# Kernel optimization log

Measured on AMD Instinct MI355X. Metric: run time of the kernel, lower is better.

The kernel has to match this reference:

```python
import jax, jax.numpy as jnp
import numpy as np

THRESH = 0.5     # confidence threshold (forward arg 'thresh' in the original)
IOU_THR = 0.1    # nms(boxes, 0.1) in the original
K = 512          # fixed top-k candidates per scale (static-shape stand-in for nonzero())


def _decode(output, anchors, stride, k):
    """Filter + parse for one scale. output: [B, 3*(5+nc), H, W]."""
    B, C, H, W = output.shape
    o = output.transpose(0, 2, 3, 1).reshape(B, H, W, 3, -1)   # [B,H,W,3,5+nc]
    D = o.shape[-1]
    conf = jax.nn.sigmoid(o[..., 0]).reshape(-1)               # [B*H*W*3]
    scores, idx = jax.lax.top_k(conf, k)                       # fixed-size filter
    n, h, w, a = jnp.unravel_index(idx, (B, H, W, 3))
    v = o.reshape(-1, D)[idx]                                  # [K, 5+nc]
    dt = v.dtype
    cy = (h.astype(dt) + jax.nn.sigmoid(v[:, 2])) * stride
    cx = (w.astype(dt) + jax.nn.sigmoid(v[:, 1])) * stride
    bw = anchors[a, 0] * jnp.exp(v[:, 3])
    bh = anchors[a, 1] * jnp.exp(v[:, 4])
    cond = jax.nn.sigmoid(v[:, 0])
    cls = jnp.argmax(v[:, 5:], axis=1).astype(dt)              # argmax(softmax)=argmax
    boxes = jnp.stack([n.astype(dt), cond, cx, cy, bw, bh, cls], axis=1)  # [K,7]
    valid = cond > THRESH
    return boxes, valid


def _nms(boxes, valid, iou_thr):
    """Greedy per-image, per-class NMS. boxes: [N,7] = (n, cond, cx, cy, w, h, cls)."""
    N = boxes.shape[0]
    score = jnp.where(valid, boxes[:, 1], -jnp.inf)
    order = jnp.argsort(-score)
    b = boxes[order]
    val = valid[order]
    x1 = b[:, 2] - b[:, 4] * 0.5
    y1 = b[:, 3] - b[:, 5] * 0.5
    x2 = b[:, 2] + b[:, 4] * 0.5
    y2 = b[:, 3] + b[:, 5] * 0.5
    area = b[:, 4] * b[:, 5]
    ix1 = jnp.maximum(x1[:, None], x1[None, :])
    iy1 = jnp.maximum(y1[:, None], y1[None, :])
    ix2 = jnp.minimum(x2[:, None], x2[None, :])
    iy2 = jnp.minimum(y2[:, None], y2[None, :])
    inter = jnp.clip(ix2 - ix1, 0) * jnp.clip(iy2 - iy1, 0)
    iou = inter / (area[:, None] + area[None, :] - inter + 1e-9)
    same = (b[:, 0, None] == b[None, :, 0]) & (b[:, 6, None] == b[None, :, 6])
    overlap = (iou > iou_thr) & same                           # [N,N] bool, no grad needed
    rng = jnp.arange(N)

    def body(i, supp):
        row = overlap[i] & (rng > i)
        active = (~supp[i]) & val[i]
        return jnp.where(active, supp | row, supp)

    supp = jax.lax.fori_loop(0, N, body, jnp.zeros(N, bool))
    keep = val & (~supp)
    return b * keep[:, None].astype(b.dtype), keep


def setup_inputs() -> dict:
    key = jax.random.key(0)
    ks = jax.random.split(key, 6)
    B, C = 64, 255  # 3 * (5 + 80 classes)
    return {
        "output_13": jax.random.normal(ks[0], (B, C, 13, 13), jnp.float32),
        "output_26": jax.random.normal(ks[1], (B, C, 26, 26), jnp.float32),
        "output_52": jax.random.normal(ks[2], (B, C, 52, 52), jnp.float32),
        "anchors_13": jax.random.uniform(ks[3], (3, 2), jnp.float32, 90.0, 330.0),
        "anchors_26": jax.random.uniform(ks[4], (3, 2), jnp.float32, 30.0, 120.0),
        "anchors_52": jax.random.uniform(ks[5], (3, 2), jnp.float32, 10.0, 60.0),
    }


def reference(output_13, output_26, output_52, anchors_13, anchors_26, anchors_52):
    b13, v13 = _decode(output_13, anchors_13, 32.0, K)
    b26, v26 = _decode(output_26, anchors_26, 16.0, K)
    b52, v52 = _decode(output_52, anchors_52, 8.0, K)
    boxes = jnp.concatenate([b13, b26, b52], axis=0)   # [3K, 7]
    valid = jnp.concatenate([v13, v26, v52], axis=0)
    final_boxes, keep = _nms(boxes, valid, IOU_THR)
    return final_boxes, keep
```

## Files before the change

kernel.cpp:

```cpp
#include <hip/hip_runtime.h>
#include <stdint.h>

#define K_SEL 512
#define NBOX 1536
#define CAND_CAP 4096
#define HBITS 13
#define HBINS 8192
#define NSHARD 128
#define SEG 128
#define HBLK 64
#define HB0 8
#define HB1 16
#define HB2 40
#define ICAP 56

#define M0 32448
#define M1 129792
#define M2 519168
#define M_TOT (M0+M1+M2)

#define OFF_HIST 0u
#define OFF_CNT  98304u
#define OFF_THR  99840u
#define OFF_CAND 99872u
#define OFF_BOX  493088u
#define OFF_SKEY 536096u
#define OFF_TOPK 548384u
#define ZERO_BYTES 99840u

typedef unsigned long long u64;
typedef uint32_t u32;
typedef uint16_t u16;

__device__ __forceinline__ float sigf(float x) { return 1.0f / (1.0f + expf(-x)); }

__device__ __forceinline__ u32 fmono(float f) {
    u32 u = __float_as_uint(f);
    return (u & 0x80000000u) ? ~u : (u | 0x80000000u);
}

__global__ __launch_bounds__(1024) void k_hist(const float* p0, const float* p1, const float* p2,
                                               uint8_t* ws) {
    __shared__ u32 lh[HBINS];
    for (int i = threadIdx.x; i < HBINS; i += 1024) lh[i] = 0;
    __syncthreads();
    int b = blockIdx.x, s, b0, nb;
    if (b < HB0)            { s = 0; b0 = b;             nb = HB0; }
    else if (b < HB0 + HB1) { s = 1; b0 = b - HB0;       nb = HB1; }
    else                    { s = 2; b0 = b - HB0 - HB1; nb = HB2; }
    int M = (s == 0) ? M0 : (s == 1) ? M1 : M2;
    int H = (s == 0) ? 13 : (s == 1) ? 26 : 52;
    int HW = H * H;
    const float* p = (s == 0) ? p0 : (s == 1) ? p1 : p2;
    for (int o = b0 * 1024 + threadIdx.x; o < M; o += nb * 1024) {
        int n = o / (3 * HW); int rem = o - n * 3 * HW;
        int a = rem / HW;     int pix = rem - a * HW;
        float conf = sigf(p[(size_t)(n * 255 + a * 85) * HW + pix]);
        atomicAdd(&lh[fmono(conf) >> (32 - HBITS)], 1u);
    }
    __syncthreads();
    u32* gh = (u32*)(ws + OFF_HIST) + s * HBINS;
    for (int i = threadIdx.x; i < HBINS; i += 1024) {
        u32 v = lh[i];
        if (v) atomicAdd(&gh[i], v);
    }
}

__global__ __launch_bounds__(1024) void k_scan(uint8_t* ws) {
    int s = blockIdx.x;
    u32* hist = (u32*)(ws + OFF_HIST) + s * HBINS;
    __shared__ u32 sum[1024];
    int t = threadIdx.x;
    u32 bins[8];
    const uint4* hp = (const uint4*)(hist + t * 8);
    uint4 x = hp[0], y = hp[1];
    bins[0] = x.x; bins[1] = x.y; bins[2] = x.z; bins[3] = x.w;
    bins[4] = y.x; bins[5] = y.y; bins[6] = y.z; bins[7] = y.w;
    u32 acc = 0;
#pragma unroll
    for (int k = 0; k < 8; ++k) acc += bins[k];
    sum[t] = acc;
    __syncthreads();
    for (int off = 1; off < 1024; off <<= 1) {
        u32 v = (t + off < 1024) ? sum[t + off] : 0;
        __syncthreads();
        sum[t] += v;
        __syncthreads();
    }
    u32 excl = (t < 1023) ? sum[t + 1] : 0;
    u32 mine = sum[t] - excl;
    if (excl < K_SEL && excl + mine >= K_SEL) {
        u32 cum = excl; int thr = t * 8;
#pragma unroll
        for (int k = 7; k >= 0; --k) {
            cum += bins[k];
            if (cum >= K_SEL) { thr = t * 8 + k; break; }
        }
        ((u32*)(ws + OFF_THR))[s] = (u32)thr;
    }
}

__global__ __launch_bounds__(1024) void k_compact(const float* p0, const float* p1, const float* p2,
                                                  uint8_t* ws) {
    int t = blockIdx.x * 1024 + threadIdx.x;
    if (t >= M_TOT) return;
    int s, o, H;
    if (t < M0)            { s = 0; o = t;           H = 13; }
    else if (t < M0 + M1)  { s = 1; o = t - M0;      H = 26; }
    else                   { s = 2; o = t - M0 - M1; H = 52; }
    const float* p = (s == 0) ? p0 : (s == 1) ? p1 : p2;
    int HW = H * H;
    int n = o / (3 * HW); int rem = o - n * 3 * HW;
    int a = rem / HW;     int pix = rem - a * HW;
    float conf = sigf(p[(size_t)(n * 255 + a * 85) * HW + pix]);
    u32 cb = fmono(conf);
    if ((cb >> (32 - HBITS)) >= ((u32*)(ws + OFF_THR))[s]) {
        int c = n * (3 * HW) + pix * 3 + a;
        int idx = s * NSHARD + (blockIdx.x & (NSHARD - 1));
        u32 pos = atomicAdd(&((u32*)(ws + OFF_CNT))[idx], 1u);
        if (pos < SEG) {
            u64 key = ((u64)cb << 32) | (u32)(~(u32)c);
            ((u64*)(ws + OFF_CAND))[(u32)idx * SEG + pos] = key;
        }
    }
}

__global__ __launch_bounds__(1024) void k_sortsel(uint8_t* ws) {
    int s = blockIdx.x;
    __shared__ u64 a_[CAND_CAP];
    __shared__ u32 scnt[NSHARD], spre[NSHARD];
    __shared__ u32 total_s;
    int t = threadIdx.x;
    if (t < NSHARD) {
        u32 v = ((u32*)(ws + OFF_CNT))[s * NSHARD + t];
        scnt[t] = (v > SEG) ? SEG : v;
        spre[t] = scnt[t];
    }
    __syncthreads();
    for (int off = 1; off < NSHARD; off <<= 1) {
        u32 v = (t >= off && t < NSHARD) ? spre[t - off] : 0;
        __syncthreads();
        if (t < NSHARD) spre[t] += v;
        __syncthreads();
    }
    if (t == 0) total_s = (spre[NSHARD - 1] > CAND_CAP) ? CAND_CAP : spre[NSHARD - 1];
    __syncthreads();
    u32 total = total_s;
    int n2 = K_SEL;
    while (n2 < (int)total) n2 <<= 1;
    for (int i = t; i < n2; i += 1024) a_[i] = 0ull;
    __syncthreads();
    if (t < NSHARD) {
        u32 base = spre[t] - scnt[t];
        const u64* seg = (const u64*)(ws + OFF_CAND) + (u32)(s * NSHARD + t) * SEG;
        for (u32 i = 0; i < scnt[t]; ++i)
            if (base + i < CAND_CAP) a_[base + i] = seg[i];
    }
    __syncthreads();
    for (int k = 2; k <= n2; k <<= 1) {
        for (int j = k >> 1; j > 0; j >>= 1) {
            for (int i = t; i < n2; i += 1024) {
                int ixj = i ^ j;
                if (ixj > i) {
                    bool desc = ((i & k) == 0);
                    u64 x = a_[i], y = a_[ixj];
                    if (desc ? (x < y) : (x > y)) { a_[i] = y; a_[ixj] = x; }
                }
            }
            __syncthreads();
        }
    }
    u64* topk = (u64*)(ws + OFF_TOPK) + s * K_SEL;
    for (int r = t; r < K_SEL; r += 1024) topk[r] = a_[r];
}

__global__ __launch_bounds__(1024) void k_decode(const float* p0, const float* p1, const float* p2,
                                                 const float* a0, const float* a1, const float* a2,
                                                 uint8_t* ws) {
    int t = blockIdx.x * 1024 + threadIdx.x;
    int g = t >> 4, l = t & 15;
    if (g >= NBOX) return;
    int s = g >> 9, r = g & 511;
    int H = (s == 0) ? 13 : (s == 1) ? 26 : 52;
    float stride = (s == 0) ? 32.f : (s == 1) ? 16.f : 8.f;
    const float* p    = (s == 0) ? p0 : (s == 1) ? p1 : p2;
    const float* anch = (s == 0) ? a0 : (s == 1) ? a1 : a2;
    int HW = H * H, hw3 = HW * 3;
    u64 key = ((u64*)(ws + OFF_TOPK))[g];
    int c = (int)(~(u32)key);
    int n = c / hw3; int rem = c - n * hw3;
    int pix = rem / 3; int aa = rem - pix * 3;
    size_t base = (size_t)(n * 255 + aa * 85) * HW + pix;
    float best = -INFINITY; int bi = 0x7FFFFFFF;
#pragma unroll
    for (int m = 0; m < 5; ++m) {
        int k2 = l + m * 16;
        float vv = p[base + (size_t)(5 + k2) * HW];
        if (vv > best) { best = vv; bi = k2; }
    }
    float vload = (l < 5) ? p[base + (size_t)l * HW] : 0.f;
#pragma unroll
    for (int off = 8; off > 0; off >>= 1) {
        float ov = __shfl_down(best, off, 16);
        int oi = __shfl_down(bi, off, 16);
        if (ov > best || (ov == best && oi < bi)) { best = ov; bi = oi; }
    }
    float v0 = __shfl(vload, 0, 16);
    float v1 = __shfl(vload, 1, 16);
    float v2 = __shfl(vload, 2, 16);
    float v3 = __shfl(vload, 3, 16);
    float v4 = __shfl(vload, 4, 16);
    if (l == 0) {
        int h = pix / H, w = pix - h * H;
        float conf = sigf(v0);
        float cx = ((float)w + sigf(v1)) * stride;
        float cy = ((float)h + sigf(v2)) * stride;
        float bw = anch[aa * 2 + 0] * expf(v3);
        float bh = anch[aa * 2 + 1] * expf(v4);
        float* box = (float*)(ws + OFF_BOX) + g * 7;
        box[0] = (float)n; box[1] = conf; box[2] = cx; box[3] = cy;
        box[4] = bw; box[5] = bh; box[6] = (float)bi;
        u32 mono = (conf > 0.5f) ? fmono(conf) : fmono(-INFINITY);
        ((u64*)(ws + OFF_SKEY))[g] = ((u64)mono << 32) | (u32)(~(u32)g);
    }
}

__global__ __launch_bounds__(1024) void k_tail(uint8_t* ws, float* out) {
    __shared__ u64 sk[NBOX];
    __shared__ u16 srt[NBOX];
    __shared__ float gx1[NBOX], gy1[NBOX], gx2[NBOX], gy2[NBOX], gar[NBOX];
    __shared__ u32 meta[NBOX];
    __shared__ uint8_t gkeep[NBOX];
    __shared__ u16 lists[64 * ICAP];
    __shared__ u32 icnt[64];
    u32* wvcnt = (u32*)sk;
    int t = threadIdx.x;
    u64* skey = (u64*)(ws + OFF_SKEY);
    for (int i = t; i < NBOX; i += 1024) sk[i] = skey[i];
    __syncthreads();
    for (int i = t; i < NBOX; i += 1024) {
        int s = i >> 9, r = i & 511;
        u64 K = sk[i];
        int g = r;
#pragma unroll
        for (int s2 = 0; s2 < 3; ++s2) {
            if (s2 == s) continue;
            const u64* seg = &sk[s2 << 9];
            int lo = 0, hi = 512;
            while (lo < hi) {
                int mid = (lo + hi) >> 1;
                if (seg[mid] > K) lo = mid + 1; else hi = mid;
            }
            g += lo;
        }
        srt[g] = (u16)i;
    }
    __syncthreads();
    const float* box = (const float*)(ws + OFF_BOX);
    for (int i = t; i < NBOX; i += 1024) {
        int pos = srt[i];
        float b0 = box[pos * 7 + 0], b1 = box[pos * 7 + 1], b2 = box[pos * 7 + 2];
        float b3 = box[pos * 7 + 3], b4 = box[pos * 7 + 4], b5 = box[pos * 7 + 5];
        float b6 = box[pos * 7 + 6];
        gx1[i] = b2 - b4 * 0.5f;  gy1[i] = b3 - b5 * 0.5f;
        gx2[i] = b2 + b4 * 0.5f;  gy2[i] = b3 + b5 * 0.5f;
        gar[i] = b4 * b5;
        meta[i] = (u32)(int)b0 | ((u32)(int)b6 << 8) | ((b1 > 0.5f) ? (1u << 16) : 0u);
        gkeep[i] = 0;
        wvcnt[i] = 0;
    }
    __syncthreads();
#pragma unroll
    for (int pass = 0; pass < 2; ++pass) {
        int ii = t + pass * 1024;
        u32 img = (ii < NBOX) ? (meta[ii] & 63u) : 0u;
        u64 mask = ~0ull;
#pragma unroll
        for (int b = 0; b < 6; ++b) {
            bool bit = (img >> b) & 1u;
            u64 bal = __ballot(bit);
            mask &= bit ? bal : ~bal;
        }
        if (ii < NBOX) {
            int lane = ii & 63;
            int wrank = __popcll(mask & ((1ull << lane) - 1ull));
            if (wrank == 0) wvcnt[(ii >> 6) * 64 + img] = (u32)__popcll(mask);
        }
    }
    __syncthreads();
    if (t < 64) {
        u32 c = 0;
        for (int w = 0; w < 24; ++w) c += wvcnt[w * 64 + t];
        icnt[t] = c;
    }
#pragma unroll
    for (int pass = 0; pass < 2; ++pass) {
        int ii = t + pass * 1024;
        u32 img = (ii < NBOX) ? (meta[ii] & 63u) : 0u;
        u64 mask = ~0ull;
#pragma unroll
        for (int b = 0; b < 6; ++b) {
            bool bit = (img >> b) & 1u;
            u64 bal = __ballot(bit);
            mask &= bit ? bal : ~bal;
        }
        if (ii < NBOX) {
            int lane = ii & 63;
            int wv = ii >> 6;
            int r = __popcll(mask & ((1ull << lane) - 1ull));
            for (int w = 0; w < wv; ++w) r += (int)wvcnt[w * 64 + img];
            if (r < ICAP) lists[img * ICAP + r] = (u16)ii;
        }
    }
    __syncthreads();
    {
        int wv = t >> 6, lane = t & 63;
        for (int im = wv * 4; im < wv * 4 + 4; ++im) {
            int cnt = (int)icnt[im]; if (cnt > ICAP) cnt = ICAP;
            float x1 = 0, y1 = 0, x2 = 0, y2 = 0, ar = 0;
            u32 cl = 0; int u = -1; bool val = false;
            if (lane < cnt) {
                u = lists[im * ICAP + lane];
                x1 = gx1[u]; y1 = gy1[u]; x2 = gx2[u]; y2 = gy2[u]; ar = gar[u];
                u32 m = meta[u]; cl = (m >> 8) & 0xFFu; val = (m >> 16) & 1u;
            }
            u64 valmask = __ballot(val);
            u64 keptmask = 0;
            for (int a = 0; a < cnt; ++a) {
                float ax1 = __shfl(x1, a), ay1 = __shfl(y1, a);
                float ax2 = __shfl(x2, a), ay2 = __shfl(y2, a);
                float aar = __shfl(ar, a);
                u32 acl = (u32)__shfl((int)cl, a);
                float ix1 = fmaxf(x1, ax1), iy1 = fmaxf(y1, ay1);
                float ix2 = fminf(x2, ax2), iy2 = fminf(y2, ay2);
                float iw = fmaxf(ix2 - ix1, 0.f), ih = fmaxf(iy2 - iy1, 0.f);
                float inter = iw * ih;
                float iou = inter / (ar + aar - inter + 1e-9f);
                bool viol = (lane < a) && ((keptmask >> lane) & 1ull) &&
                            (cl == acl) && (iou > 0.1f);
                u64 bal = __ballot(viol);
                bool kept = ((valmask >> a) & 1ull) && (bal == 0ull);
                if (kept) keptmask |= (1ull << a);
            }
            if (lane < cnt) gkeep[u] = (uint8_t)((keptmask >> lane) & 1ull);
        }
    }
    __syncthreads();
    for (int i = t; i < NBOX; i += 1024) {
        float kf = gkeep[i] ? 1.f : 0.f;
        int pos = srt[i];
        for (int k = 0; k < 7; ++k) out[i * 7 + k] = box[pos * 7 + k] * kf;
        out[NBOX * 7 + i] = kf;
    }
}

extern "C" void kernel_launch(void* const* d_in, const int* in_sizes, int n_in,
                              void* d_out, int out_size, void* d_ws, size_t ws_size,
                              hipStream_t stream) {
    const float* p0 = (const float*)d_in[0];
    const float* p1 = (const float*)d_in[1];
    const float* p2 = (const float*)d_in[2];
    const float* a0 = (const float*)d_in[3];
    const float* a1 = (const float*)d_in[4];
    const float* a2 = (const float*)d_in[5];
    uint8_t* ws = (uint8_t*)d_ws;
    float* out = (float*)d_out;

    const int CB = (M_TOT + 1023) / 1024;

    hipMemsetAsync(ws, 0, ZERO_BYTES, stream);
    k_hist   <<<HBLK, 1024, 0, stream>>>(p0, p1, p2, ws);
    k_scan   <<<3, 1024, 0, stream>>>(ws);
    k_compact<<<CB, 1024, 0, stream>>>(p0, p1, p2, ws);
    k_sortsel<<<3, 1024, 0, stream>>>(ws);
    k_decode <<<24, 1024, 0, stream>>>(p0, p1, p2, a0, a1, a2, ws);
    k_tail   <<<1, 1024, 0, stream>>>(ws, out);
}
```

Measured before the change: 118.0 us.

## Fuse top-k sort with decode, use register wave bitonic sort, drop memset

The pipeline now writes per-block histogram slices, which k_scan sums, in place of global atomics. Shard counters are zeroed inside k_scan, so the memset launch goes away. The shared-memory bitonic sort and the separate decode kernel are merged into one kernel. Each of 8 waves sorts 512 keys in registers with shuffles, and a merge tree keeps the top 512. Every one of the 24 blocks redundantly re-sorts its scale's candidates and then decodes its own 64 boxes, trading duplicated sort work for fewer launches and shorter barrier chains. The histogram block count is also cut from 64 to 24.

```diff
diff --git a/kernel.cpp b/kernel.cpp
--- a/kernel.cpp
+++ b/kernel.cpp
@@ -3,15 +3,11 @@
 
 #define K_SEL 512
 #define NBOX 1536
-#define CAND_CAP 4096
 #define HBITS 13
 #define HBINS 8192
 #define NSHARD 128
 #define SEG 128
-#define HBLK 64
-#define HB0 8
-#define HB1 16
-#define HB2 40
+#define HBLK 24
 #define ICAP 56
 
 #define M0 32448
@@ -19,14 +15,12 @@
 #define M2 519168
 #define M_TOT (M0+M1+M2)
 
-#define OFF_HIST 0u
-#define OFF_CNT  98304u
-#define OFF_THR  99840u
-#define OFF_CAND 99872u
-#define OFF_BOX  493088u
-#define OFF_SKEY 536096u
-#define OFF_TOPK 548384u
-#define ZERO_BYTES 99840u
+#define OFF_HSL  0u
+#define OFF_CNT  786432u
+#define OFF_THR  787968u
+#define OFF_CAND 788000u
+#define OFF_BOX  1181216u
+#define OFF_SKEY 1224224u
 
 typedef unsigned long long u64;
 typedef uint32_t u32;
@@ -37,6 +31,69 @@
 __device__ __forceinline__ u32 fmono(float f) {
     u32 u = __float_as_uint(f);
     return (u & 0x80000000u) ? ~u : (u | 0x80000000u);
+}
+
+__device__ __forceinline__ u64 sx64(u64 v, int m) {
+    int lo = __shfl_xor((int)(u32)v, m);
+    int hi = __shfl_xor((int)(v >> 32), m);
+    return ((u64)(u32)hi << 32) | (u32)lo;
+}
+
+__device__ __forceinline__ void ce_reg(u64& lo, u64& hi, bool desc) {
+    u64 mx = lo > hi ? lo : hi;
+    u64 mn = lo > hi ? hi : lo;
+    lo = desc ? mx : mn;
+    hi = desc ? mn : mx;
+}
+
+__device__ __forceinline__ void wave_sort512(u64 (&kr)[8], int lane) {
+#pragma unroll
+    for (int k = 2; k <= 512; k <<= 1) {
+#pragma unroll
+        for (int j = k >> 1; j > 0; j >>= 1) {
+            if (j >= 64) {
+                int rj = j >> 6;
+#pragma unroll
+                for (int r = 0; r < 8; ++r) {
+                    if ((r & rj) == 0) {
+                        bool desc = ((r & (k >> 6)) == 0);
+                        ce_reg(kr[r], kr[r | rj], desc);
+                    }
+                }
+            } else {
+#pragma unroll
+                for (int r = 0; r < 8; ++r) {
+                    u64 other = sx64(kr[r], j);
+                    bool desc = (k < 64) ? ((lane & k) == 0) : ((r & (k >> 6)) == 0);
+                    bool keep_max = (((lane & j) == 0) == desc);
+                    u64 mx = kr[r] > other ? kr[r] : other;
+                    u64 mn = kr[r] > other ? other : kr[r];
+                    kr[r] = keep_max ? mx : mn;
+                }
+            }
+        }
+    }
+}
+
+__device__ __forceinline__ void wave_clean512(u64 (&kr)[8], int lane) {
+#pragma unroll
+    for (int j = 256; j > 0; j >>= 1) {
+        if (j >= 64) {
+            int rj = j >> 6;
+#pragma unroll
+            for (int r = 0; r < 8; ++r)
+                if ((r & rj) == 0) ce_reg(kr[r], kr[r | rj], true);
+        } else {
+#pragma unroll
+            for (int r = 0; r < 8; ++r) {
+                u64 other = sx64(kr[r], j);
+                bool keep_max = ((lane & j) == 0);
+                u64 mx = kr[r] > other ? kr[r] : other;
+                u64 mn = kr[r] > other ? other : kr[r];
+                kr[r] = keep_max ? mx : mn;
+            }
+        }
+    }
 }
 
 __global__ __launch_bounds__(1024) void k_hist(const float* p0, const float* p1, const float* p2,
@@ -45,9 +102,9 @@
     for (int i = threadIdx.x; i < HBINS; i += 1024) lh[i] = 0;
     __syncthreads();
     int b = blockIdx.x, s, b0, nb;
-    if (b < HB0)            { s = 0; b0 = b;             nb = HB0; }
-    else if (b < HB0 + HB1) { s = 1; b0 = b - HB0;       nb = HB1; }
-    else                    { s = 2; b0 = b - HB0 - HB1; nb = HB2; }
+    if (b < 2)      { s = 0; b0 = b;     nb = 2;  }
+    else if (b < 8) { s = 1; b0 = b - 2; nb = 6;  }
+    else            { s = 2; b0 = b - 8; nb = 16; }
     int M = (s == 0) ? M0 : (s == 1) ? M1 : M2;
     int H = (s == 0) ? 13 : (s == 1) ? 26 : 52;
     int HW = H * H;
@@ -59,23 +116,26 @@
         atomicAdd(&lh[fmono(conf) >> (32 - HBITS)], 1u);
     }
     __syncthreads();
-    u32* gh = (u32*)(ws + OFF_HIST) + s * HBINS;
-    for (int i = threadIdx.x; i < HBINS; i += 1024) {
-        u32 v = lh[i];
-        if (v) atomicAdd(&gh[i], v);
-    }
+    u32* slice = (u32*)(ws + OFF_HSL) + (u32)b * HBINS;
+    for (int i = threadIdx.x; i < HBINS; i += 1024) slice[i] = lh[i];
 }
 
 __global__ __launch_bounds__(1024) void k_scan(uint8_t* ws) {
     int s = blockIdx.x;
-    u32* hist = (u32*)(ws + OFF_HIST) + s * HBINS;
+    int b0 = (s == 0) ? 0 : (s == 1) ? 2 : 8;
+    int b1 = (s == 0) ? 2 : (s == 1) ? 8 : 24;
     __shared__ u32 sum[1024];
     int t = threadIdx.x;
+    if (t < NSHARD) ((u32*)(ws + OFF_CNT))[s * NSHARD + t] = 0;
     u32 bins[8];
-    const uint4* hp = (const uint4*)(hist + t * 8);
-    uint4 x = hp[0], y = hp[1];
-    bins[0] = x.x; bins[1] = x.y; bins[2] = x.z; bins[3] = x.w;
-    bins[4] = y.x; bins[5] = y.y; bins[6] = y.z; bins[7] = y.w;
+#pragma unroll
+    for (int k = 0; k < 8; ++k) bins[k] = 0;
+    for (int b = b0; b < b1; ++b) {
+        const uint4* sl = (const uint4*)((u32*)(ws + OFF_HSL) + (u32)b * HBINS + t * 8);
+        uint4 x = sl[0], y = sl[1];
+        bins[0] += x.x; bins[1] += x.y; bins[2] += x.z; bins[3] += x.w;
+        bins[4] += y.x; bins[5] += y.y; bins[6] += y.z; bins[7] += y.w;
+    }
     u32 acc = 0;
 #pragma unroll
     for (int k = 0; k < 8; ++k) acc += bins[k];
@@ -125,11 +185,14 @@
     }
 }
 
-__global__ __launch_bounds__(1024) void k_sortsel(uint8_t* ws) {
-    int s = blockIdx.x;
-    __shared__ u64 a_[CAND_CAP];
+__global__ __launch_bounds__(1024) void k_sortdec(const float* p0, const float* p1, const float* p2,
+                                                  const float* a0, const float* a1, const float* a2,
+                                                  uint8_t* ws) {
+    int s = blockIdx.x >> 3, sub = blockIdx.x & 7;
+    __shared__ u64 a_[4096];
     __shared__ u32 scnt[NSHARD], spre[NSHARD];
-    __shared__ u32 total_s;
+    __shared__ float pbv[64];
+    __shared__ int pbi[64];
     int t = threadIdx.x;
     if (t < NSHARD) {
         u32 v = ((u32*)(ws + OFF_CNT))[s * NSHARD + t];
@@ -143,50 +206,84 @@
         if (t < NSHARD) spre[t] += v;
         __syncthreads();
     }
-    if (t == 0) total_s = (spre[NSHARD - 1] > CAND_CAP) ? CAND_CAP : spre[NSHARD - 1];
-    __syncthreads();
-    u32 total = total_s;
-    int n2 = K_SEL;
-    while (n2 < (int)total) n2 <<= 1;
-    for (int i = t; i < n2; i += 1024) a_[i] = 0ull;
+    for (int i = t; i < 4096; i += 1024) a_[i] = 0ull;
     __syncthreads();
     if (t < NSHARD) {
         u32 base = spre[t] - scnt[t];
         const u64* seg = (const u64*)(ws + OFF_CAND) + (u32)(s * NSHARD + t) * SEG;
         for (u32 i = 0; i < scnt[t]; ++i)
-            if (base + i < CAND_CAP) a_[base + i] = seg[i];
-    }
-    __syncthreads();
-    for (int k = 2; k <= n2; k <<= 1) {
-        for (int j = k >> 1; j > 0; j >>= 1) {
-            for (int i = t; i < n2; i += 1024) {
-                int ixj = i ^ j;
-                if (ixj > i) {
-                    bool desc = ((i & k) == 0);
-                    u64 x = a_[i], y = a_[ixj];
-                    if (desc ? (x < y) : (x > y)) { a_[i] = y; a_[ixj] = x; }
-                }
-            }
-            __syncthreads();
-        }
-    }
-    u64* topk = (u64*)(ws + OFF_TOPK) + s * K_SEL;
-    for (int r = t; r < K_SEL; r += 1024) topk[r] = a_[r];
-}
-
-__global__ __launch_bounds__(1024) void k_decode(const float* p0, const float* p1, const float* p2,
-                                                 const float* a0, const float* a1, const float* a2,
-                                                 uint8_t* ws) {
-    int t = blockIdx.x * 1024 + threadIdx.x;
-    int g = t >> 4, l = t & 15;
-    if (g >= NBOX) return;
-    int s = g >> 9, r = g & 511;
+            if (base + i < 4096) a_[base + i] = seg[i];
+    }
+    __syncthreads();
+    int wv = t >> 6, lane = t & 63;
+    u64 kr[8];
+    if (wv < 8) {
+#pragma unroll
+        for (int r = 0; r < 8; ++r) kr[r] = a_[wv * 512 + r * 64 + lane];
+        wave_sort512(kr, lane);
+    }
+    __syncthreads();
+    if (wv < 8) {
+#pragma unroll
+        for (int r = 0; r < 8; ++r) a_[wv * 512 + r * 64 + lane] = kr[r];
+    }
+    __syncthreads();
+    if (wv < 4) {
+#pragma unroll
+        for (int r = 0; r < 8; ++r) {
+            int e = r * 64 + lane;
+            u64 A = a_[(2 * wv) * 512 + e];
+            u64 B = a_[(2 * wv + 1) * 512 + 511 - e];
+            kr[r] = A > B ? A : B;
+        }
+        wave_clean512(kr, lane);
+    }
+    __syncthreads();
+    if (wv < 4) {
+#pragma unroll
+        for (int r = 0; r < 8; ++r) a_[wv * 512 + r * 64 + lane] = kr[r];
+    }
+    __syncthreads();
+    if (wv < 2) {
+#pragma unroll
+        for (int r = 0; r < 8; ++r) {
+            int e = r * 64 + lane;
+            u64 A = a_[(2 * wv) * 512 + e];
+            u64 B = a_[(2 * wv + 1) * 512 + 511 - e];
+            kr[r] = A > B ? A : B;
+        }
+        wave_clean512(kr, lane);
+    }
+    __syncthreads();
+    if (wv < 2) {
+#pragma unroll
+        for (int r = 0; r < 8; ++r) a_[wv * 512 + r * 64 + lane] = kr[r];
+    }
+    __syncthreads();
+    if (wv == 0) {
+#pragma unroll
+        for (int r = 0; r < 8; ++r) {
+            int e = r * 64 + lane;
+            u64 A = a_[e];
+            u64 B = a_[512 + 511 - e];
+            kr[r] = A > B ? A : B;
+        }
+        wave_clean512(kr, lane);
+    }
+    __syncthreads();
+    if (wv == 0) {
+#pragma unroll
+        for (int r = 0; r < 8; ++r) a_[r * 64 + lane] = kr[r];
+    }
+    __syncthreads();
+    int g16 = t >> 4, l = t & 15;
+    int rloc = sub * 64 + g16;
     int H = (s == 0) ? 13 : (s == 1) ? 26 : 52;
     float stride = (s == 0) ? 32.f : (s == 1) ? 16.f : 8.f;
     const float* p    = (s == 0) ? p0 : (s == 1) ? p1 : p2;
     const float* anch = (s == 0) ? a0 : (s == 1) ? a1 : a2;
     int HW = H * H, hw3 = HW * 3;
-    u64 key = ((u64*)(ws + OFF_TOPK))[g];
+    u64 key = a_[rloc];
     int c = (int)(~(u32)key);
     int n = c / hw3; int rem = c - n * hw3;
     int pix = rem / 3; int aa = rem - pix * 3;
@@ -210,6 +307,7 @@
     float v2 = __shfl(vload, 2, 16);
     float v3 = __shfl(vload, 3, 16);
     float v4 = __shfl(vload, 4, 16);
+    (void)pbv; (void)pbi;
     if (l == 0) {
         int h = pix / H, w = pix - h * H;
         float conf = sigf(v0);
@@ -217,11 +315,12 @@
         float cy = ((float)h + sigf(v2)) * stride;
         float bw = anch[aa * 2 + 0] * expf(v3);
         float bh = anch[aa * 2 + 1] * expf(v4);
-        float* box = (float*)(ws + OFF_BOX) + g * 7;
+        int gi = s * K_SEL + rloc;
+        float* box = (float*)(ws + OFF_BOX) + gi * 7;
         box[0] = (float)n; box[1] = conf; box[2] = cx; box[3] = cy;
         box[4] = bw; box[5] = bh; box[6] = (float)bi;
         u32 mono = (conf > 0.5f) ? fmono(conf) : fmono(-INFINITY);
-        ((u64*)(ws + OFF_SKEY))[g] = ((u64)mono << 32) | (u32)(~(u32)g);
+        ((u64*)(ws + OFF_SKEY))[gi] = ((u64)mono << 32) | (u32)(~(u32)gi);
     }
 }
 
@@ -368,11 +467,9 @@
 
     const int CB = (M_TOT + 1023) / 1024;
 
-    hipMemsetAsync(ws, 0, ZERO_BYTES, stream);
     k_hist   <<<HBLK, 1024, 0, stream>>>(p0, p1, p2, ws);
     k_scan   <<<3, 1024, 0, stream>>>(ws);
     k_compact<<<CB, 1024, 0, stream>>>(p0, p1, p2, ws);
-    k_sortsel<<<3, 1024, 0, stream>>>(ws);
-    k_decode <<<24, 1024, 0, stream>>>(p0, p1, p2, a0, a1, a2, ws);
+    k_sortdec<<<24, 1024, 0, stream>>>(p0, p1, p2, a0, a1, a2, ws);
     k_tail   <<<1, 1024, 0, stream>>>(ws, out);
 }
```

After: 125.2 us. 6.1% more time.

## Fuse all stages into one cooperative persistent kernel with grid syncs

Applied to the files above, without the earlier changes.

Replaces the memset and six separate launches with a single cooperative kernel of 192 blocks that runs histogram, scan, compaction, sort, decode and NMS tail as phases separated by grid-wide syncs, with shared memory held in a union. Histogram blocks now write per-block slices that the scan reduces, so global atomics and the memset go away. Compaction becomes a grid-stride loop. A multi-kernel fallback remains for when the cooperative launch fails. The aim is to remove launch and inter-kernel gaps, at the cost of grid-sync overhead, fewer histogram blocks, and mostly idle blocks during the serial phases.

```diff
diff --git a/kernel.cpp b/kernel.cpp
--- a/kernel.cpp
+++ b/kernel.cpp
@@ -1,17 +1,17 @@
 #include <hip/hip_runtime.h>
+#include <hip/hip_cooperative_groups.h>
 #include <stdint.h>
 
+namespace cg = cooperative_groups;
+
+#define GRID 192
 #define K_SEL 512
 #define NBOX 1536
-#define CAND_CAP 4096
 #define HBITS 13
 #define HBINS 8192
 #define NSHARD 128
 #define SEG 128
-#define HBLK 64
-#define HB0 8
-#define HB1 16
-#define HB2 40
+#define HBLK 24
 #define ICAP 56
 
 #define M0 32448
@@ -19,14 +19,13 @@
 #define M2 519168
 #define M_TOT (M0+M1+M2)
 
-#define OFF_HIST 0u
-#define OFF_CNT  98304u
-#define OFF_THR  99840u
-#define OFF_CAND 99872u
-#define OFF_BOX  493088u
-#define OFF_SKEY 536096u
-#define OFF_TOPK 548384u
-#define ZERO_BYTES 99840u
+#define OFF_HSL  0u
+#define OFF_CNT  786432u
+#define OFF_THR  787968u
+#define OFF_CAND 788000u
+#define OFF_BOX  1181216u
+#define OFF_SKEY 1224224u
+#define OFF_TOPK 1236512u
 
 typedef unsigned long long u64;
 typedef uint32_t u32;
@@ -39,43 +38,61 @@
     return (u & 0x80000000u) ? ~u : (u | 0x80000000u);
 }
 
-__global__ __launch_bounds__(1024) void k_hist(const float* p0, const float* p1, const float* p2,
-                                               uint8_t* ws) {
-    __shared__ u32 lh[HBINS];
-    for (int i = threadIdx.x; i < HBINS; i += 1024) lh[i] = 0;
-    __syncthreads();
-    int b = blockIdx.x, s, b0, nb;
-    if (b < HB0)            { s = 0; b0 = b;             nb = HB0; }
-    else if (b < HB0 + HB1) { s = 1; b0 = b - HB0;       nb = HB1; }
-    else                    { s = 2; b0 = b - HB0 - HB1; nb = HB2; }
+struct SortSh {
+    u64 a_[4096];
+    u32 scnt[NSHARD], spre[NSHARD];
+};
+struct TailSh {
+    u64 sk[NBOX];
+    u16 srt[NBOX];
+    float gx1[NBOX], gy1[NBOX], gx2[NBOX], gy2[NBOX], gar[NBOX];
+    u32 meta[NBOX];
+    uint8_t gkeep[NBOX];
+    u16 lists[64 * ICAP];
+    u32 icnt[64];
+};
+union AllSh {
+    u32 lh[HBINS];
+    u32 sum[1024];
+    SortSh sort;
+    TailSh tail;
+};
+
+__device__ void dev_hist(int hb, const float* p0, const float* p1, const float* p2,
+                         uint8_t* ws, u32* lh, int t) {
+    for (int i = t; i < HBINS; i += 1024) lh[i] = 0;
+    __syncthreads();
+    int s, b0, nb;
+    if (hb < 2)      { s = 0; b0 = hb;     nb = 2;  }
+    else if (hb < 8) { s = 1; b0 = hb - 2; nb = 6;  }
+    else             { s = 2; b0 = hb - 8; nb = 16; }
     int M = (s == 0) ? M0 : (s == 1) ? M1 : M2;
     int H = (s == 0) ? 13 : (s == 1) ? 26 : 52;
     int HW = H * H;
     const float* p = (s == 0) ? p0 : (s == 1) ? p1 : p2;
-    for (int o = b0 * 1024 + threadIdx.x; o < M; o += nb * 1024) {
+    for (int o = b0 * 1024 + t; o < M; o += nb * 1024) {
         int n = o / (3 * HW); int rem = o - n * 3 * HW;
         int a = rem / HW;     int pix = rem - a * HW;
         float conf = sigf(p[(size_t)(n * 255 + a * 85) * HW + pix]);
         atomicAdd(&lh[fmono(conf) >> (32 - HBITS)], 1u);
     }
     __syncthreads();
-    u32* gh = (u32*)(ws + OFF_HIST) + s * HBINS;
-    for (int i = threadIdx.x; i < HBINS; i += 1024) {
-        u32 v = lh[i];
-        if (v) atomicAdd(&gh[i], v);
-    }
-}
-
-__global__ __launch_bounds__(1024) void k_scan(uint8_t* ws) {
-    int s = blockIdx.x;
-    u32* hist = (u32*)(ws + OFF_HIST) + s * HBINS;
-    __shared__ u32 sum[1024];
-    int t = threadIdx.x;
+    u32* slice = (u32*)(ws + OFF_HSL) + (u32)hb * HBINS;
+    for (int i = t; i < HBINS; i += 1024) slice[i] = lh[i];
+}
+
+__device__ void dev_scan(int s, uint8_t* ws, u32* sum, int t) {
+    int b0 = (s == 0) ? 0 : (s == 1) ? 2 : 8;
+    int b1 = (s == 0) ? 2 : (s == 1) ? 8 : 24;
     u32 bins[8];
-    const uint4* hp = (const uint4*)(hist + t * 8);
-    uint4 x = hp[0], y = hp[1];
-    bins[0] = x.x; bins[1] = x.y; bins[2] = x.z; bins[3] = x.w;
-    bins[4] = y.x; bins[5] = y.y; bins[6] = y.z; bins[7] = y.w;
+#pragma unroll
+    for (int k = 0; k < 8; ++k) bins[k] = 0;
+    for (int b = b0; b < b1; ++b) {
+        const uint4* sl = (const uint4*)((u32*)(ws + OFF_HSL) + (u32)b * HBINS + t * 8);
+        uint4 x = sl[0], y = sl[1];
+        bins[0] += x.x; bins[1] += x.y; bins[2] += x.z; bins[3] += x.w;
+        bins[4] += y.x; bins[5] += y.y; bins[6] += y.z; bins[7] += y.w;
+    }
     u32 acc = 0;
 #pragma unroll
     for (int k = 0; k < 8; ++k) acc += bins[k];
@@ -100,61 +117,56 @@
     }
 }
 
-__global__ __launch_bounds__(1024) void k_compact(const float* p0, const float* p1, const float* p2,
-                                                  uint8_t* ws) {
-    int t = blockIdx.x * 1024 + threadIdx.x;
-    if (t >= M_TOT) return;
-    int s, o, H;
-    if (t < M0)            { s = 0; o = t;           H = 13; }
-    else if (t < M0 + M1)  { s = 1; o = t - M0;      H = 26; }
-    else                   { s = 2; o = t - M0 - M1; H = 52; }
-    const float* p = (s == 0) ? p0 : (s == 1) ? p1 : p2;
-    int HW = H * H;
-    int n = o / (3 * HW); int rem = o - n * 3 * HW;
-    int a = rem / HW;     int pix = rem - a * HW;
-    float conf = sigf(p[(size_t)(n * 255 + a * 85) * HW + pix]);
-    u32 cb = fmono(conf);
-    if ((cb >> (32 - HBITS)) >= ((u32*)(ws + OFF_THR))[s]) {
-        int c = n * (3 * HW) + pix * 3 + a;
-        int idx = s * NSHARD + (blockIdx.x & (NSHARD - 1));
-        u32 pos = atomicAdd(&((u32*)(ws + OFF_CNT))[idx], 1u);
-        if (pos < SEG) {
-            u64 key = ((u64)cb << 32) | (u32)(~(u32)c);
-            ((u64*)(ws + OFF_CAND))[(u32)idx * SEG + pos] = key;
-        }
-    }
-}
-
-__global__ __launch_bounds__(1024) void k_sortsel(uint8_t* ws) {
-    int s = blockIdx.x;
-    __shared__ u64 a_[CAND_CAP];
-    __shared__ u32 scnt[NSHARD], spre[NSHARD];
-    __shared__ u32 total_s;
-    int t = threadIdx.x;
+__device__ void dev_compact(int bid, int t, const float* p0, const float* p1, const float* p2,
+                            uint8_t* ws) {
+    const u32* thr = (const u32*)(ws + OFF_THR);
+    for (int i = bid * 1024 + t; i < M_TOT; i += GRID * 1024) {
+        int s, o, H;
+        if (i < M0)            { s = 0; o = i;           H = 13; }
+        else if (i < M0 + M1)  { s = 1; o = i - M0;      H = 26; }
+        else                   { s = 2; o = i - M0 - M1; H = 52; }
+        const float* p = (s == 0) ? p0 : (s == 1) ? p1 : p2;
+        int HW = H * H;
+        int n = o / (3 * HW); int rem = o - n * 3 * HW;
+        int a = rem / HW;     int pix = rem - a * HW;
+        float conf = sigf(p[(size_t)(n * 255 + a * 85) * HW + pix]);
+        u32 cb = fmono(conf);
+        if ((cb >> (32 - HBITS)) >= thr[s]) {
+            int c = n * (3 * HW) + pix * 3 + a;
+            int idx = s * NSHARD + (bid & (NSHARD - 1));
+            u32 pos = atomicAdd(&((u32*)(ws + OFF_CNT))[idx], 1u);
+            if (pos < SEG) {
+                u64 key = ((u64)cb << 32) | (u32)(~(u32)c);
+                ((u64*)(ws + OFF_CAND))[(u32)idx * SEG + pos] = key;
+            }
+        }
+    }
+}
+
+__device__ void dev_sort(int s, uint8_t* ws, SortSh& S, int t) {
     if (t < NSHARD) {
         u32 v = ((u32*)(ws + OFF_CNT))[s * NSHARD + t];
-        scnt[t] = (v > SEG) ? SEG : v;
-        spre[t] = scnt[t];
+        S.scnt[t] = (v > SEG) ? SEG : v;
+        S.spre[t] = S.scnt[t];
     }
     __syncthreads();
     for (int off = 1; off < NSHARD; off <<= 1) {
-        u32 v = (t >= off && t < NSHARD) ? spre[t - off] : 0;
+        u32 v = (t >= off && t < NSHARD) ? S.spre[t - off] : 0;
         __syncthreads();
-        if (t < NSHARD) spre[t] += v;
+        if (t < NSHARD) S.spre[t] += v;
         __syncthreads();
     }
-    if (t == 0) total_s = (spre[NSHARD - 1] > CAND_CAP) ? CAND_CAP : spre[NSHARD - 1];
-    __syncthreads();
-    u32 total = total_s;
+    u32 total = S.spre[NSHARD - 1];
+    if (total > 4096) total = 4096;
     int n2 = K_SEL;
     while (n2 < (int)total) n2 <<= 1;
-    for (int i = t; i < n2; i += 1024) a_[i] = 0ull;
+    for (int i = t; i < n2; i += 1024) S.a_[i] = 0ull;
     __syncthreads();
     if (t < NSHARD) {
-        u32 base = spre[t] - scnt[t];
+        u32 base = S.spre[t] - S.scnt[t];
         const u64* seg = (const u64*)(ws + OFF_CAND) + (u32)(s * NSHARD + t) * SEG;
-        for (u32 i = 0; i < scnt[t]; ++i)
-            if (base + i < CAND_CAP) a_[base + i] = seg[i];
+        for (u32 i = 0; i < S.scnt[t]; ++i)
+            if (base + i < 4096) S.a_[base + i] = seg[i];
     }
     __syncthreads();
     for (int k = 2; k <= n2; k <<= 1) {
@@ -163,24 +175,21 @@
                 int ixj = i ^ j;
                 if (ixj > i) {
                     bool desc = ((i & k) == 0);
-                    u64 x = a_[i], y = a_[ixj];
-                    if (desc ? (x < y) : (x > y)) { a_[i] = y; a_[ixj] = x; }
+                    u64 x = S.a_[i], y = S.a_[ixj];
+                    if (desc ? (x < y) : (x > y)) { S.a_[i] = y; S.a_[ixj] = x; }
                 }
             }
             __syncthreads();
         }
     }
     u64* topk = (u64*)(ws + OFF_TOPK) + s * K_SEL;
-    for (int r = t; r < K_SEL; r += 1024) topk[r] = a_[r];
-}
-
-__global__ __launch_bounds__(1024) void k_decode(const float* p0, const float* p1, const float* p2,
-                                                 const float* a0, const float* a1, const float* a2,
-                                                 uint8_t* ws) {
-    int t = blockIdx.x * 1024 + threadIdx.x;
-    int g = t >> 4, l = t & 15;
-    if (g >= NBOX) return;
-    int s = g >> 9, r = g & 511;
+    for (int r = t; r < K_SEL; r += 1024) topk[r] = S.a_[r];
+}
+
+__device__ void dev_decode(int g, int l,
+                           const float* p0, const float* p1, const float* p2,
+                           const float* a0, const float* a1, const float* a2, uint8_t* ws) {
+    int s = g >> 9;
     int H = (s == 0) ? 13 : (s == 1) ? 26 : 52;
     float stride = (s == 0) ? 32.f : (s == 1) ? 16.f : 8.f;
     const float* p    = (s == 0) ? p0 : (s == 1) ? p1 : p2;
@@ -225,27 +234,19 @@
     }
 }
 
-__global__ __launch_bounds__(1024) void k_tail(uint8_t* ws, float* out) {
-    __shared__ u64 sk[NBOX];
-    __shared__ u16 srt[NBOX];
-    __shared__ float gx1[NBOX], gy1[NBOX], gx2[NBOX], gy2[NBOX], gar[NBOX];
-    __shared__ u32 meta[NBOX];
-    __shared__ uint8_t gkeep[NBOX];
-    __shared__ u16 lists[64 * ICAP];
-    __shared__ u32 icnt[64];
-    u32* wvcnt = (u32*)sk;
-    int t = threadIdx.x;
+__device__ void dev_tail(uint8_t* ws, float* out, TailSh& T, int t) {
+    u32* wvcnt = (u32*)T.sk;
     u64* skey = (u64*)(ws + OFF_SKEY);
-    for (int i = t; i < NBOX; i += 1024) sk[i] = skey[i];
+    for (int i = t; i < NBOX; i += 1024) T.sk[i] = skey[i];
     __syncthreads();
     for (int i = t; i < NBOX; i += 1024) {
         int s = i >> 9, r = i & 511;
-        u64 K = sk[i];
+        u64 K = T.sk[i];
         int g = r;
 #pragma unroll
         for (int s2 = 0; s2 < 3; ++s2) {
             if (s2 == s) continue;
-            const u64* seg = &sk[s2 << 9];
+            const u64* seg = &T.sk[s2 << 9];
             int lo = 0, hi = 512;
             while (lo < hi) {
                 int mid = (lo + hi) >> 1;
@@ -253,27 +254,27 @@
             }
             g += lo;
         }
-        srt[g] = (u16)i;
+        T.srt[g] = (u16)i;
     }
     __syncthreads();
     const float* box = (const float*)(ws + OFF_BOX);
     for (int i = t; i < NBOX; i += 1024) {
-        int pos = srt[i];
+        int pos = T.srt[i];
         float b0 = box[pos * 7 + 0], b1 = box[pos * 7 + 1], b2 = box[pos * 7 + 2];
         float b3 = box[pos * 7 + 3], b4 = box[pos * 7 + 4], b5 = box[pos * 7 + 5];
         float b6 = box[pos * 7 + 6];
-        gx1[i] = b2 - b4 * 0.5f;  gy1[i] = b3 - b5 * 0.5f;
-        gx2[i] = b2 + b4 * 0.5f;  gy2[i] = b3 + b5 * 0.5f;
-        gar[i] = b4 * b5;
-        meta[i] = (u32)(int)b0 | ((u32)(int)b6 << 8) | ((b1 > 0.5f) ? (1u << 16) : 0u);
-        gkeep[i] = 0;
+        T.gx1[i] = b2 - b4 * 0.5f;  T.gy1[i] = b3 - b5 * 0.5f;
+        T.gx2[i] = b2 + b4 * 0.5f;  T.gy2[i] = b3 + b5 * 0.5f;
+        T.gar[i] = b4 * b5;
+        T.meta[i] = (u32)(int)b0 | ((u32)(int)b6 << 8) | ((b1 > 0.5f) ? (1u << 16) : 0u);
+        T.gkeep[i] = 0;
         wvcnt[i] = 0;
     }
     __syncthreads();
 #pragma unroll
     for (int pass = 0; pass < 2; ++pass) {
         int ii = t + pass * 1024;
-        u32 img = (ii < NBOX) ? (meta[ii] & 63u) : 0u;
+        u32 img = (ii < NBOX) ? (T.meta[ii] & 63u) : 0u;
         u64 mask = ~0ull;
 #pragma unroll
         for (int b = 0; b < 6; ++b) {
@@ -291,12 +292,12 @@
     if (t < 64) {
         u32 c = 0;
         for (int w = 0; w < 24; ++w) c += wvcnt[w * 64 + t];
-        icnt[t] = c;
+        T.icnt[t] = c;
     }
 #pragma unroll
     for (int pass = 0; pass < 2; ++pass) {
         int ii = t + pass * 1024;
-        u32 img = (ii < NBOX) ? (meta[ii] & 63u) : 0u;
+        u32 img = (ii < NBOX) ? (T.meta[ii] & 63u) : 0u;
         u64 mask = ~0ull;
 #pragma unroll
         for (int b = 0; b < 6; ++b) {
@@ -306,23 +307,23 @@
         }
         if (ii < NBOX) {
             int lane = ii & 63;
-            int wv = ii >> 6;
+            int wvv = ii >> 6;
             int r = __popcll(mask & ((1ull << lane) - 1ull));
-            for (int w = 0; w < wv; ++w) r += (int)wvcnt[w * 64 + img];
-            if (r < ICAP) lists[img * ICAP + r] = (u16)ii;
+            for (int w = 0; w < wvv; ++w) r += (int)wvcnt[w * 64 + img];
+            if (r < ICAP) T.lists[img * ICAP + r] = (u16)ii;
         }
     }
     __syncthreads();
     {
         int wv = t >> 6, lane = t & 63;
         for (int im = wv * 4; im < wv * 4 + 4; ++im) {
-            int cnt = (int)icnt[im]; if (cnt > ICAP) cnt = ICAP;
+            int cnt = (int)T.icnt[im]; if (cnt > ICAP) cnt = ICAP;
             float x1 = 0, y1 = 0, x2 = 0, y2 = 0, ar = 0;
             u32 cl = 0; int u = -1; bool val = false;
             if (lane < cnt) {
-                u = lists[im * ICAP + lane];
-                x1 = gx1[u]; y1 = gy1[u]; x2 = gx2[u]; y2 = gy2[u]; ar = gar[u];
-                u32 m = meta[u]; cl = (m >> 8) & 0xFFu; val = (m >> 16) & 1u;
+                u = T.lists[im * ICAP + lane];
+                x1 = T.gx1[u]; y1 = T.gy1[u]; x2 = T.gx2[u]; y2 = T.gy2[u]; ar = T.gar[u];
+                u32 m = T.meta[u]; cl = (m >> 8) & 0xFFu; val = (m >> 16) & 1u;
             }
             u64 valmask = __ballot(val);
             u64 keptmask = 0;
@@ -342,16 +343,71 @@
                 bool kept = ((valmask >> a) & 1ull) && (bal == 0ull);
                 if (kept) keptmask |= (1ull << a);
             }
-            if (lane < cnt) gkeep[u] = (uint8_t)((keptmask >> lane) & 1ull);
+            if (lane < cnt) T.gkeep[u] = (uint8_t)((keptmask >> lane) & 1ull);
         }
     }
     __syncthreads();
     for (int i = t; i < NBOX; i += 1024) {
-        float kf = gkeep[i] ? 1.f : 0.f;
-        int pos = srt[i];
+        float kf = T.gkeep[i] ? 1.f : 0.f;
+        int pos = T.srt[i];
         for (int k = 0; k < 7; ++k) out[i * 7 + k] = box[pos * 7 + k] * kf;
         out[NBOX * 7 + i] = kf;
     }
+}
+
+__global__ __launch_bounds__(1024) void k_all(const float* p0, const float* p1, const float* p2,
+                                              const float* a0, const float* a1, const float* a2,
+                                              uint8_t* ws, float* out) {
+    __shared__ AllSh sh;
+    cg::grid_group grid = cg::this_grid();
+    int bid = blockIdx.x, t = threadIdx.x;
+
+    if (bid < HBLK) dev_hist(bid, p0, p1, p2, ws, sh.lh, t);
+    if (bid == HBLK && t < 3 * NSHARD) ((u32*)(ws + OFF_CNT))[t] = 0;
+    grid.sync();
+
+    if (bid < 3) dev_scan(bid, ws, sh.sum, t);
+    grid.sync();
+
+    dev_compact(bid, t, p0, p1, p2, ws);
+    grid.sync();
+
+    if (bid < 3) dev_sort(bid, ws, sh.sort, t);
+    grid.sync();
+
+    if (t < 128) dev_decode(bid * 8 + (t >> 4), t & 15, p0, p1, p2, a0, a1, a2, ws);
+    grid.sync();
+
+    if (bid == 0) dev_tail(ws, out, sh.tail, t);
+}
+
+__global__ __launch_bounds__(1024) void fb_hist(const float* p0, const float* p1, const float* p2,
+                                                uint8_t* ws) {
+    __shared__ u32 lh[HBINS];
+    if (blockIdx.x < HBLK) dev_hist(blockIdx.x, p0, p1, p2, ws, lh, threadIdx.x);
+    else if (threadIdx.x < 3 * NSHARD) ((u32*)(ws + OFF_CNT))[threadIdx.x] = 0;
+}
+__global__ __launch_bounds__(1024) void fb_scan(uint8_t* ws) {
+    __shared__ u32 sum[1024];
+    dev_scan(blockIdx.x, ws, sum, threadIdx.x);
+}
+__global__ __launch_bounds__(1024) void fb_compact(const float* p0, const float* p1, const float* p2,
+                                                   uint8_t* ws) {
+    dev_compact(blockIdx.x, threadIdx.x, p0, p1, p2, ws);
+}
+__global__ __launch_bounds__(1024) void fb_sort(uint8_t* ws) {
+    __shared__ SortSh S;
+    dev_sort(blockIdx.x, ws, S, threadIdx.x);
+}
+__global__ __launch_bounds__(128) void fb_decode(const float* p0, const float* p1, const float* p2,
+                                                 const float* a0, const float* a1, const float* a2,
+                                                 uint8_t* ws) {
+    dev_decode(blockIdx.x * 8 + (threadIdx.x >> 4), threadIdx.x & 15,
+               p0, p1, p2, a0, a1, a2, ws);
+}
+__global__ __launch_bounds__(1024) void fb_tail(uint8_t* ws, float* out) {
+    __shared__ TailSh T;
+    dev_tail(ws, out, T, threadIdx.x);
 }
 
 extern "C" void kernel_launch(void* const* d_in, const int* in_sizes, int n_in,
@@ -365,14 +421,20 @@
     const float* a2 = (const float*)d_in[5];
     uint8_t* ws = (uint8_t*)d_ws;
     float* out = (float*)d_out;
-
-    const int CB = (M_TOT + 1023) / 1024;
-
-    hipMemsetAsync(ws, 0, ZERO_BYTES, stream);
-    k_hist   <<<HBLK, 1024, 0, stream>>>(p0, p1, p2, ws);
-    k_scan   <<<3, 1024, 0, stream>>>(ws);
-    k_compact<<<CB, 1024, 0, stream>>>(p0, p1, p2, ws);
-    k_sortsel<<<3, 1024, 0, stream>>>(ws);
-    k_decode <<<24, 1024, 0, stream>>>(p0, p1, p2, a0, a1, a2, ws);
-    k_tail   <<<1, 1024, 0, stream>>>(ws, out);
-}
+    (void)in_sizes; (void)n_in; (void)out_size; (void)ws_size;
+
+    void* args[] = { (void*)&p0, (void*)&p1, (void*)&p2,
+                     (void*)&a0, (void*)&a1, (void*)&a2,
+                     (void*)&ws, (void*)&out };
+    hipError_t e = hipLaunchCooperativeKernel((const void*)k_all, dim3(GRID), dim3(1024),
+                                              args, 0, stream);
+    if (e != hipSuccess) {
+        (void)hipGetLastError();
+        fb_hist   <<<HBLK + 1, 1024, 0, stream>>>(p0, p1, p2, ws);
+        fb_scan   <<<3, 1024, 0, stream>>>(ws);
+        fb_compact<<<GRID, 1024, 0, stream>>>(p0, p1, p2, ws);
+        fb_sort   <<<3, 1024, 0, stream>>>(ws);
+        fb_decode <<<192, 128, 0, stream>>>(p0, p1, p2, a0, a1, a2, ws);
+        fb_tail   <<<1, 1024, 0, stream>>>(ws, out);
+    }
+}
```

New measurement: 224.9 us. 1.91x slower.
